# Kernel tuning notes

Measured on AMD Instinct MI355X. Metric: run time of the kernel, lower is better.

Reference implementation:

```python
import jax, jax.numpy as jnp
import numpy as np

# --- static config (matches init_kwargs) ---
B, N, M = 128, 32, 32
C_IMG, NUM_HIDDEN, NUM_CLASSES = 1, 16, 3
INPUT_DIM = C_IMG + NUM_HIDDEN + NUM_CLASSES          # 20
OUT_DIM = NUM_HIDDEN + NUM_CLASSES + 2                # 21 (moving -> 2 action channels)
C_STATE = INPUT_DIM - C_IMG                           # 19
N_NEO, M_NEO = N - 2, M - 2                           # size_neo=None -> N-2
N_ACTIVE, M_ACTIVE = N - 2, M - 2
ITERATIONS = 10
IN_FEAT = 9 * INPUT_DIM + 2                           # 182, position='current'
THRESH = 0.0007


def setup_inputs() -> dict:
    key = jax.random.key(0)
    ks = jax.random.split(key, 7)
    images = jax.random.uniform(ks[0], (B, N, M, C_IMG), dtype=jnp.float32)
    W1 = jax.random.normal(ks[1], (IN_FEAT, 30), dtype=jnp.float32) * 0.08
    b1 = jnp.zeros((30,), jnp.float32)
    W2 = jax.random.normal(ks[2], (30, 30), dtype=jnp.float32) * 0.18
    b2 = jnp.zeros((30,), jnp.float32)
    W3 = jax.random.normal(ks[3], (30, OUT_DIM), dtype=jnp.float32) * 0.18
    b3 = jnp.zeros((OUT_DIM,), jnp.float32)
    return {"images": images, "W1": W1, "b1": b1, "W2": W2, "b2": b2, "W3": W3, "b3": b3}


def _custom_round(a):
    # positive -> +1, negative -> -1 (with deadzone |a| <= 0.0007 -> 0)
    return jnp.where(a > THRESH, 1, jnp.where(a < -THRESH, -1, 0)).astype(jnp.int32)


def _run(images, W1, b1, W2, b2, W3, b3):
    dx = jnp.arange(3)
    b_idx = jnp.arange(B)[:, None, None, None, None]        # (B,1,1,1,1)
    # fixed 3x3 windows into state (comms): state[x:x+3, y:y+3]
    sr = (jnp.arange(N_NEO)[:, None] + dx)[:, None, :, None]  # (Nn,1,3,1)
    sc = (jnp.arange(M_NEO)[:, None] + dx)[None, :, None, :]  # (1,Mn,1,3)
    half_n = N // 2
    half_m = M // 2

    # initial perception matrix: identity grid (N_neo == N_active)
    gx, gy = jnp.meshgrid(jnp.arange(N_NEO), jnp.arange(M_NEO), indexing="ij")
    perc0 = jnp.broadcast_to(jnp.stack([gx, gy], -1).astype(jnp.int32), (B, N_NEO, M_NEO, 2))
    state0 = jnp.zeros((B, N, M, C_STATE), jnp.float32)
    guesses0 = jnp.zeros((B * N_NEO * M_NEO, OUT_DIM), jnp.float32)

    def step(carry, _):
        state, perc, _ = carry
        px = perc[..., 0]  # (B,Nn,Mn) int32
        py = perc[..., 1]
        # dynamic 3x3 image patches at (px, py)
        rows = px[..., None, None] + dx[:, None]            # (B,Nn,Mn,3,1)
        cols = py[..., None, None] + dx[None, :]            # (B,Nn,Mn,1,3)
        perc_patch = images[b_idx, rows, cols, :]           # (B,Nn,Mn,3,3,C_IMG)
        comms = state[:, sr, sc, :]                          # (B,Nn,Mn,3,3,C_STATE)
        feat = jnp.concatenate([perc_patch, comms], axis=-1)  # (B,Nn,Mn,3,3,INPUT_DIM)
        feat = feat.reshape(B * N_NEO * M_NEO, 9 * INPUT_DIM)
        # position='current' features
        pos_x = ((px - half_n) / half_n).astype(jnp.float32).reshape(-1, 1)
        pos_y = ((py - half_m) / half_m).astype(jnp.float32).reshape(-1, 1)
        inp = jnp.concatenate([feat, pos_x, pos_y], axis=-1)  # (B*Nn*Mn, 182)
        h = jax.nn.relu(inp @ W1 + b1)
        h = jax.nn.relu(h @ W2 + b2)
        guesses = h @ W3 + b3                                 # (B*Nn*Mn, 21)
        outputs = guesses.reshape(B, N_NEO, M_NEO, OUT_DIM)
        state = state.at[:, 1:1 + N_NEO, 1:1 + M_NEO, :].add(outputs[..., :C_STATE])
        # movement: round actions to {-1,0,1}, add, clip to [0, N_active-1]
        delta = _custom_round(outputs[..., -2:])
        perc = jnp.clip(perc + delta, 0, N_ACTIVE - 1)
        return (state, perc, guesses), None

    (state, perc, guesses), _ = jax.lax.scan(step, (state0, perc0, guesses0), None, length=ITERATIONS)
    class_state = state[:, 1:1 + N_NEO, 1:1 + M_NEO, -NUM_CLASSES:]
    return class_state, guesses


def reference(images, W1, b1, W2, b2, W3, b3):
    return _run(images, W1, b1, W2, b2, W3, b3)
```

## Files before the change

### kernel.cpp

```cpp
#include <hip/hip_runtime.h>

#define B_      128
#define NPIX    32
#define NNEO    30
#define CSTATE  19
#define CPAD    20
#define OUTD    21
#define ITERS   10
#define THRESHV 0.0007f

#define STATE_ELEMS_PAD (B_ * NPIX * NPIX * CPAD)
#define NCELLS      (B_ * NNEO * NNEO)
#define CLASS_ELEMS (NCELLS * 3)
#define HSTRIDE 31

__global__ void nca_init(float* __restrict__ stateA, float* __restrict__ stateB) {
    int idx = blockIdx.x * blockDim.x + threadIdx.x;
    const int total = B_ * 124 * CPAD;
    if (idx >= total) return;
    int c  = idx % CPAD;
    int t2 = idx / CPAD;
    int cell = t2 % 124;
    int b    = t2 / 124;
    int i, j;
    if (cell < 32)      { i = 0;  j = cell; }
    else if (cell < 64) { i = 31; j = cell - 32; }
    else { int k = cell - 64; i = 1 + (k >> 1); j = (k & 1) ? 31 : 0; }
    size_t off = (((size_t)b * NPIX + i) * NPIX + j) * CPAD + c;
    stateA[off] = 0.0f;
    stateB[off] = 0.0f;
}

__global__ __launch_bounds__(1024, 8)
void nca_step0(const float* __restrict__ img,
               const float* __restrict__ W1, const float* __restrict__ b1,
               const float* __restrict__ W2, const float* __restrict__ b2,
               const float* __restrict__ W3, const float* __restrict__ b3,
               float* __restrict__ state_new, int* __restrict__ perc) {
    __shared__ float s_img[NPIX * NPIX];
    __shared__ float s_h[240 * HSTRIDE];

    const int b   = blockIdx.y;
    const int rg  = blockIdx.x;
    const int i0  = (rg < 2) ? rg * 8 : 16 + (rg - 2) * 7;
    const int nr  = (rg < 2) ? 8 : 7;
    const int tid = threadIdx.x;
    const int qh  = __builtin_amdgcn_readfirstlane(tid >> 8);
    const int cell = tid & 255;
    const int qoff = (qh == 0) ? 0 : (qh == 1) ? 8 : (qh == 2) ? 14 : 22;
    const int off3 = 5 * qh;

    if (tid < NPIX * NPIX / 4) {
        ((float4*)s_img)[tid] = ((const float4*)(img + (size_t)b * NPIX * NPIX))[tid];
    }
    __syncthreads();

    const int cells = nr * NNEO;
    const bool active = cell < cells;

    int r = 0, j = 0, i = 0, gcell = 0, px = 0, py = 0;
    if (active) {
        r = cell / NNEO;
        j = cell % NNEO;
        i = i0 + r;
        gcell = (b * NNEO + i) * NNEO + j;
        px = i; py = j;
    }

    float h1[8];
    {
        const float* __restrict__ bb = b1 + qoff;
#pragma unroll
        for (int q = 0; q < 8; q++) h1[q] = bb[q];
    }
    if (active) {
        for (int pr = 0; pr < 3; pr++) {
            for (int pc = 0; pc < 3; pc++) {
                const int p9 = pr * 3 + pc;
                const float iv = s_img[(px + pr) * NPIX + (py + pc)];
                const float* __restrict__ wp = W1 + (p9 * 20) * 30 + qoff;
#pragma unroll
                for (int q = 0; q < 8; q++) h1[q] += iv * wp[q];
            }
        }
        const float posx = (float)(px - 16) * (1.0f / 16.0f);
        const float posy = (float)(py - 16) * (1.0f / 16.0f);
        const float* __restrict__ wx = W1 + 180 * 30 + qoff;
        const float* __restrict__ wy = W1 + 181 * 30 + qoff;
#pragma unroll
        for (int q = 0; q < 8; q++) h1[q] += posx * wx[q];
#pragma unroll
        for (int q = 0; q < 8; q++) h1[q] += posy * wy[q];
#pragma unroll
        for (int q = 0; q < 8; q++) h1[q] = fmaxf(h1[q], 0.0f);
#pragma unroll
        for (int q = 0; q < 8; q++) s_h[cell * HSTRIDE + qoff + q] = h1[q];
    }
    __syncthreads();

    float h2[8];
    {
        const float* __restrict__ bb = b2 + qoff;
#pragma unroll
        for (int q = 0; q < 8; q++) h2[q] = bb[q];
    }
    if (active) {
        float a1[30];
#pragma unroll
        for (int k = 0; k < 30; k++) a1[k] = s_h[cell * HSTRIDE + k];
        for (int k = 0; k < 30; k++) {
            const float* __restrict__ wr = W2 + k * 30 + qoff;
#pragma unroll
            for (int q = 0; q < 8; q++) h2[q] += a1[k] * wr[q];
        }
#pragma unroll
        for (int q = 0; q < 8; q++) h2[q] = fmaxf(h2[q], 0.0f);
    }
    __syncthreads();
    if (active) {
#pragma unroll
        for (int q = 0; q < 8; q++) s_h[cell * HSTRIDE + qoff + q] = h2[q];
    }
    __syncthreads();

    float o[6];
    {
        const float* __restrict__ bb = b3 + off3;
#pragma unroll
        for (int c = 0; c < 6; c++) o[c] = bb[c];
    }
    if (active) {
        float a2[30];
#pragma unroll
        for (int k = 0; k < 30; k++) a2[k] = s_h[cell * HSTRIDE + k];
        for (int k = 0; k < 30; k++) {
            const float* __restrict__ wr = W3 + k * 21 + off3;
#pragma unroll
            for (int c = 0; c < 6; c++) o[c] += a2[k] * wr[c];
        }
        float* __restrict__ ns =
            state_new + (((size_t)b * NPIX + (i + 1)) * NPIX + (j + 1)) * CPAD;
        if (qh == 0) {
#pragma unroll
            for (int c = 0; c < 6; c++) ns[c] = o[c];
        } else if (qh < 3) {
#pragma unroll
            for (int c = 1; c < 6; c++) ns[off3 + c] = o[c];
        } else {
#pragma unroll
            for (int c = 1; c < 4; c++) ns[15 + c] = o[c];
            int dxm = (o[4] > THRESHV) ? 1 : ((o[4] < -THRESHV) ? -1 : 0);
            int dym = (o[5] > THRESHV) ? 1 : ((o[5] < -THRESHV) ? -1 : 0);
            px += dxm; py += dym;
            px = (px < 0) ? 0 : ((px > NNEO - 1) ? NNEO - 1 : px);
            py = (py < 0) ? 0 : ((py > NNEO - 1) ? NNEO - 1 : py);
            perc[2 * gcell + 0] = px;
            perc[2 * gcell + 1] = py;
        }
    }
}

template<bool LAST>
__global__ __launch_bounds__(1024, 8)
void nca_step(const float* __restrict__ img,
              const float* __restrict__ W1, const float* __restrict__ b1,
              const float* __restrict__ W2, const float* __restrict__ b2,
              const float* __restrict__ W3, const float* __restrict__ b3,
              const float* __restrict__ state_old, float* __restrict__ state_new,
              int* perc, float* __restrict__ guesses_out,
              float* __restrict__ class_out) {
    __shared__ float s_state[10 * NPIX * CPAD];
    __shared__ float s_img[NPIX * NPIX];
    __shared__ float s_h[240 * HSTRIDE];

    const int b   = blockIdx.y;
    const int rg  = blockIdx.x;
    const int i0  = (rg < 2) ? rg * 8 : 16 + (rg - 2) * 7;
    const int nr  = (rg < 2) ? 8 : 7;
    const int tid = threadIdx.x;
    const int qh  = __builtin_amdgcn_readfirstlane(tid >> 8);
    const int cell = tid & 255;
    const int qoff = (qh == 0) ? 0 : (qh == 1) ? 8 : (qh == 2) ? 14 : 22;
    const int off3 = 5 * qh;

    {
        const int n4 = (nr + 2) * NPIX * CPAD / 4;
        const float4* gstate4 =
            (const float4*)(state_old + ((size_t)b * NPIX + i0) * NPIX * CPAD);
        float4* s_state4 = (float4*)s_state;
        for (int t = tid; t < n4; t += 1024) s_state4[t] = gstate4[t];
    }
    if (tid < NPIX * NPIX / 4) {
        ((float4*)s_img)[tid] = ((const float4*)(img + (size_t)b * NPIX * NPIX))[tid];
    }
    __syncthreads();

    const int cells = nr * NNEO;
    const bool active = cell < cells;

    int r = 0, j = 0, i = 0, gcell = 0, px = 0, py = 0;
    if (active) {
        r = cell / NNEO;
        j = cell % NNEO;
        i = i0 + r;
        gcell = (b * NNEO + i) * NNEO + j;
        px = perc[2 * gcell]; py = perc[2 * gcell + 1];
    }

    float h1[8];
    {
        const float* __restrict__ bb = b1 + qoff;
#pragma unroll
        for (int q = 0; q < 8; q++) h1[q] = bb[q];
    }
    if (active) {
        for (int pr = 0; pr < 3; pr++) {
            for (int pc = 0; pc < 3; pc++) {
                const int p9 = pr * 3 + pc;
                const float iv = s_img[(px + pr) * NPIX + (py + pc)];
                const float* __restrict__ wp = W1 + (p9 * 20) * 30 + qoff;
                const int sbase = ((r + pr) * NPIX + (j + pc)) * CPAD;
                float fv[20];
                {
                    const float4* __restrict__ sp =
                        (const float4*)&s_state[sbase];
#pragma unroll
                    for (int v = 0; v < 5; v++)
                        *(float4*)&fv[4 * v] = sp[v];
                }
#pragma unroll
                for (int q = 0; q < 8; q++) h1[q] += iv * wp[q];
                for (int ch = 0; ch < CSTATE; ch++) {
                    const float* __restrict__ wr = wp + (ch + 1) * 30;
#pragma unroll
                    for (int q = 0; q < 8; q++) h1[q] += fv[ch] * wr[q];
                }
            }
        }
        const float posx = (float)(px - 16) * (1.0f / 16.0f);
        const float posy = (float)(py - 16) * (1.0f / 16.0f);
        const float* __restrict__ wx = W1 + 180 * 30 + qoff;
        const float* __restrict__ wy = W1 + 181 * 30 + qoff;
#pragma unroll
        for (int q = 0; q < 8; q++) h1[q] += posx * wx[q];
#pragma unroll
        for (int q = 0; q < 8; q++) h1[q] += posy * wy[q];
#pragma unroll
        for (int q = 0; q < 8; q++) h1[q] = fmaxf(h1[q], 0.0f);
#pragma unroll
        for (int q = 0; q < 8; q++) s_h[cell * HSTRIDE + qoff + q] = h1[q];
    }
    __syncthreads();

    float h2[8];
    {
        const float* __restrict__ bb = b2 + qoff;
#pragma unroll
        for (int q = 0; q < 8; q++) h2[q] = bb[q];
    }
    if (active) {
        float a1[30];
#pragma unroll
        for (int k = 0; k < 30; k++) a1[k] = s_h[cell * HSTRIDE + k];
        for (int k = 0; k < 30; k++) {
            const float* __restrict__ wr = W2 + k * 30 + qoff;
#pragma unroll
            for (int q = 0; q < 8; q++) h2[q] += a1[k] * wr[q];
        }
#pragma unroll
        for (int q = 0; q < 8; q++) h2[q] = fmaxf(h2[q], 0.0f);
    }
    __syncthreads();
    if (active) {
#pragma unroll
        for (int q = 0; q < 8; q++) s_h[cell * HSTRIDE + qoff + q] = h2[q];
    }
    __syncthreads();

    float o[6];
    {
        const float* __restrict__ bb = b3 + off3;
#pragma unroll
        for (int c = 0; c < 6; c++) o[c] = bb[c];
    }
    if (active) {
        float a2[30];
#pragma unroll
        for (int k = 0; k < 30; k++) a2[k] = s_h[cell * HSTRIDE + k];
        for (int k = 0; k < 30; k++) {
            const float* __restrict__ wr = W3 + k * 21 + off3;
#pragma unroll
            for (int c = 0; c < 6; c++) o[c] += a2[k] * wr[c];
        }

        const int lcenter = ((r + 1) * NPIX + (j + 1)) * CPAD;
        if (!LAST) {
            float* __restrict__ ns =
                state_new + (((size_t)b * NPIX + (i + 1)) * NPIX + (j + 1)) * CPAD;
            if (qh == 0) {
#pragma unroll
                for (int c = 0; c < 6; c++)
                    ns[c] = s_state[lcenter + c] + o[c];
            } else if (qh < 3) {
#pragma unroll
                for (int c = 1; c < 6; c++)
                    ns[off3 + c] = s_state[lcenter + off3 + c] + o[c];
            } else {
#pragma unroll
                for (int c = 1; c < 4; c++)
                    ns[15 + c] = s_state[lcenter + 15 + c] + o[c];
                int dxm = (o[4] > THRESHV) ? 1 : ((o[4] < -THRESHV) ? -1 : 0);
                int dym = (o[5] > THRESHV) ? 1 : ((o[5] < -THRESHV) ? -1 : 0);
                px += dxm; py += dym;
                px = (px < 0) ? 0 : ((px > NNEO - 1) ? NNEO - 1 : px);
                py = (py < 0) ? 0 : ((py > NNEO - 1) ? NNEO - 1 : py);
                perc[2 * gcell + 0] = px;
                perc[2 * gcell + 1] = py;
            }
        } else {
            float* __restrict__ g = guesses_out + (size_t)gcell * OUTD;
            if (qh == 0) {
#pragma unroll
                for (int c = 0; c < 6; c++) g[c] = o[c];
            } else {
#pragma unroll
                for (int c = 1; c < 6; c++) g[off3 + c] = o[c];
            }
            if (qh == 3) {
                float* __restrict__ cs = class_out + (size_t)gcell * 3;
#pragma unroll
                for (int cc = 0; cc < 3; cc++)
                    cs[cc] = s_state[lcenter + 16 + cc] + o[1 + cc];
            }
        }
    }
}

extern "C" void kernel_launch(void* const* d_in, const int* in_sizes, int n_in,
                              void* d_out, int out_size, void* d_ws, size_t ws_size,
                              hipStream_t stream) {
    const float* img = (const float*)d_in[0];
    const float* W1  = (const float*)d_in[1];
    const float* b1  = (const float*)d_in[2];
    const float* W2  = (const float*)d_in[3];
    const float* b2  = (const float*)d_in[4];
    const float* W3  = (const float*)d_in[5];
    const float* b3  = (const float*)d_in[6];

    float* out = (float*)d_out;
    float* class_out   = out;
    float* guesses_out = out + CLASS_ELEMS;

    float* stateA = (float*)d_ws;
    float* stateB = stateA + STATE_ELEMS_PAD;
    int*   perc   = (int*)(stateB + STATE_ELEMS_PAD);

    {
        const int total = B_ * 124 * CPAD;
        nca_init<<<(total + 255) / 256, 256, 0, stream>>>(stateA, stateB);
    }

    const dim3 grid(4, B_);
    nca_step0<<<grid, 1024, 0, stream>>>(img, W1, b1, W2, b2, W3, b3,
                                         stateB, perc);
    for (int t = 1; t < ITERS - 1; t++) {
        const float* so = (t & 1) ? stateB : stateA;
        float*       sn = (t & 1) ? stateA : stateB;
        nca_step<false><<<grid, 1024, 0, stream>>>(
            img, W1, b1, W2, b2, W3, b3, so, sn, perc, guesses_out, class_out);
    }
    nca_step<true><<<grid, 1024, 0, stream>>>(
        img, W1, b1, W2, b2, W3, b3, stateB, stateA, perc, guesses_out, class_out);
}
```

Baseline: 346.9 us.

## Compute full MLP per thread, one cell per thread, drop shared memory

Replaces the 1024-thread blocks, which split each cell's 30 hidden units across four thread groups with shared-memory exchange and barriers, by a one-thread-per-cell kernel that computes all 30/30/21 outputs in registers. State windows are read straight from global memory as float4 rather than staged in LDS. Weights are read uniformly from global or scalar memory. This removes the barriers and shared-memory traffic, but raises register pressure to about 90 accumulators per thread and issues redundant overlapping global loads of neighbouring state.

After: 482.7 us. 1.39x slower.

```diff
diff --git a/kernel.cpp b/kernel.cpp
--- a/kernel.cpp
+++ b/kernel.cpp
@@ -12,7 +12,6 @@
 #define STATE_ELEMS_PAD (B_ * NPIX * NPIX * CPAD)
 #define NCELLS      (B_ * NNEO * NNEO)
 #define CLASS_ELEMS (NCELLS * 3)
-#define HSTRIDE 31
 
 __global__ void nca_init(float* __restrict__ stateA, float* __restrict__ stateB) {
     int idx = blockIdx.x * blockDim.x + threadIdx.x;
@@ -20,319 +19,137 @@
     if (idx >= total) return;
     int c  = idx % CPAD;
     int t2 = idx / CPAD;
-    int cell = t2 % 124;
+    int cellp = t2 % 124;
     int b    = t2 / 124;
     int i, j;
-    if (cell < 32)      { i = 0;  j = cell; }
-    else if (cell < 64) { i = 31; j = cell - 32; }
-    else { int k = cell - 64; i = 1 + (k >> 1); j = (k & 1) ? 31 : 0; }
+    if (cellp < 32)      { i = 0;  j = cellp; }
+    else if (cellp < 64) { i = 31; j = cellp - 32; }
+    else { int k = cellp - 64; i = 1 + (k >> 1); j = (k & 1) ? 31 : 0; }
     size_t off = (((size_t)b * NPIX + i) * NPIX + j) * CPAD + c;
     stateA[off] = 0.0f;
     stateB[off] = 0.0f;
 }
 
-__global__ __launch_bounds__(1024, 8)
-void nca_step0(const float* __restrict__ img,
-               const float* __restrict__ W1, const float* __restrict__ b1,
-               const float* __restrict__ W2, const float* __restrict__ b2,
-               const float* __restrict__ W3, const float* __restrict__ b3,
-               float* __restrict__ state_new, int* __restrict__ perc) {
-    __shared__ float s_img[NPIX * NPIX];
-    __shared__ float s_h[240 * HSTRIDE];
+#define L1ROW(x, r) do { const float* __restrict__ wr = wp + (r) * 30; \
+    _Pragma("unroll") for (int o = 0; o < 30; o++) acc[o] += (x) * wr[o]; } while (0)
 
-    const int b   = blockIdx.y;
-    const int rg  = blockIdx.x;
-    const int i0  = (rg < 2) ? rg * 8 : 16 + (rg - 2) * 7;
-    const int nr  = (rg < 2) ? 8 : 7;
-    const int tid = threadIdx.x;
-    const int qh  = __builtin_amdgcn_readfirstlane(tid >> 8);
-    const int cell = tid & 255;
-    const int qoff = (qh == 0) ? 0 : (qh == 1) ? 8 : (qh == 2) ? 14 : 22;
-    const int off3 = 5 * qh;
-
-    if (tid < NPIX * NPIX / 4) {
-        ((float4*)s_img)[tid] = ((const float4*)(img + (size_t)b * NPIX * NPIX))[tid];
-    }
-    __syncthreads();
-
-    const int cells = nr * NNEO;
-    const bool active = cell < cells;
-
-    int r = 0, j = 0, i = 0, gcell = 0, px = 0, py = 0;
-    if (active) {
-        r = cell / NNEO;
-        j = cell % NNEO;
-        i = i0 + r;
-        gcell = (b * NNEO + i) * NNEO + j;
-        px = i; py = j;
-    }
-
-    float h1[8];
-    {
-        const float* __restrict__ bb = b1 + qoff;
-#pragma unroll
-        for (int q = 0; q < 8; q++) h1[q] = bb[q];
-    }
-    if (active) {
-        for (int pr = 0; pr < 3; pr++) {
-            for (int pc = 0; pc < 3; pc++) {
-                const int p9 = pr * 3 + pc;
-                const float iv = s_img[(px + pr) * NPIX + (py + pc)];
-                const float* __restrict__ wp = W1 + (p9 * 20) * 30 + qoff;
-#pragma unroll
-                for (int q = 0; q < 8; q++) h1[q] += iv * wp[q];
-            }
-        }
-        const float posx = (float)(px - 16) * (1.0f / 16.0f);
-        const float posy = (float)(py - 16) * (1.0f / 16.0f);
-        const float* __restrict__ wx = W1 + 180 * 30 + qoff;
-        const float* __restrict__ wy = W1 + 181 * 30 + qoff;
-#pragma unroll
-        for (int q = 0; q < 8; q++) h1[q] += posx * wx[q];
-#pragma unroll
-        for (int q = 0; q < 8; q++) h1[q] += posy * wy[q];
-#pragma unroll
-        for (int q = 0; q < 8; q++) h1[q] = fmaxf(h1[q], 0.0f);
-#pragma unroll
-        for (int q = 0; q < 8; q++) s_h[cell * HSTRIDE + qoff + q] = h1[q];
-    }
-    __syncthreads();
-
-    float h2[8];
-    {
-        const float* __restrict__ bb = b2 + qoff;
-#pragma unroll
-        for (int q = 0; q < 8; q++) h2[q] = bb[q];
-    }
-    if (active) {
-        float a1[30];
-#pragma unroll
-        for (int k = 0; k < 30; k++) a1[k] = s_h[cell * HSTRIDE + k];
-        for (int k = 0; k < 30; k++) {
-            const float* __restrict__ wr = W2 + k * 30 + qoff;
-#pragma unroll
-            for (int q = 0; q < 8; q++) h2[q] += a1[k] * wr[q];
-        }
-#pragma unroll
-        for (int q = 0; q < 8; q++) h2[q] = fmaxf(h2[q], 0.0f);
-    }
-    __syncthreads();
-    if (active) {
-#pragma unroll
-        for (int q = 0; q < 8; q++) s_h[cell * HSTRIDE + qoff + q] = h2[q];
-    }
-    __syncthreads();
-
-    float o[6];
-    {
-        const float* __restrict__ bb = b3 + off3;
-#pragma unroll
-        for (int c = 0; c < 6; c++) o[c] = bb[c];
-    }
-    if (active) {
-        float a2[30];
-#pragma unroll
-        for (int k = 0; k < 30; k++) a2[k] = s_h[cell * HSTRIDE + k];
-        for (int k = 0; k < 30; k++) {
-            const float* __restrict__ wr = W3 + k * 21 + off3;
-#pragma unroll
-            for (int c = 0; c < 6; c++) o[c] += a2[k] * wr[c];
-        }
-        float* __restrict__ ns =
-            state_new + (((size_t)b * NPIX + (i + 1)) * NPIX + (j + 1)) * CPAD;
-        if (qh == 0) {
-#pragma unroll
-            for (int c = 0; c < 6; c++) ns[c] = o[c];
-        } else if (qh < 3) {
-#pragma unroll
-            for (int c = 1; c < 6; c++) ns[off3 + c] = o[c];
-        } else {
-#pragma unroll
-            for (int c = 1; c < 4; c++) ns[15 + c] = o[c];
-            int dxm = (o[4] > THRESHV) ? 1 : ((o[4] < -THRESHV) ? -1 : 0);
-            int dym = (o[5] > THRESHV) ? 1 : ((o[5] < -THRESHV) ? -1 : 0);
-            px += dxm; py += dym;
-            px = (px < 0) ? 0 : ((px > NNEO - 1) ? NNEO - 1 : px);
-            py = (py < 0) ? 0 : ((py > NNEO - 1) ? NNEO - 1 : py);
-            perc[2 * gcell + 0] = px;
-            perc[2 * gcell + 1] = py;
-        }
-    }
-}
-
-template<bool LAST>
-__global__ __launch_bounds__(1024, 8)
-void nca_step(const float* __restrict__ img,
+template<int MODE>
+__global__ __launch_bounds__(256, 2)
+void nca_cell(const float* __restrict__ img,
               const float* __restrict__ W1, const float* __restrict__ b1,
               const float* __restrict__ W2, const float* __restrict__ b2,
               const float* __restrict__ W3, const float* __restrict__ b3,
               const float* __restrict__ state_old, float* __restrict__ state_new,
-              int* perc, float* __restrict__ guesses_out,
-              float* __restrict__ class_out) {
-    __shared__ float s_state[10 * NPIX * CPAD];
-    __shared__ float s_img[NPIX * NPIX];
-    __shared__ float s_h[240 * HSTRIDE];
+              int* __restrict__ perc,
+              float* __restrict__ guesses_out, float* __restrict__ class_out)
+{
+    const int cell = blockIdx.x * 256 + threadIdx.x;
+    const int b  = cell / (NNEO * NNEO);
+    const int ij = cell - b * (NNEO * NNEO);
+    const int i  = ij / NNEO;
+    const int j  = ij - i * NNEO;
 
-    const int b   = blockIdx.y;
-    const int rg  = blockIdx.x;
-    const int i0  = (rg < 2) ? rg * 8 : 16 + (rg - 2) * 7;
-    const int nr  = (rg < 2) ? 8 : 7;
-    const int tid = threadIdx.x;
-    const int qh  = __builtin_amdgcn_readfirstlane(tid >> 8);
-    const int cell = tid & 255;
-    const int qoff = (qh == 0) ? 0 : (qh == 1) ? 8 : (qh == 2) ? 14 : 22;
-    const int off3 = 5 * qh;
+    int px, py;
+    if (MODE == 0) { px = i; py = j; }
+    else           { px = perc[2 * cell]; py = perc[2 * cell + 1]; }
 
+    const float* __restrict__ ib = img + (size_t)b * (NPIX * NPIX);
+
+    float acc[30];
+#pragma unroll
+    for (int o = 0; o < 30; o++) acc[o] = b1[o];
+
+#pragma clang loop unroll(disable)
+    for (int pr = 0; pr < 3; pr++) {
+#pragma clang loop unroll(disable)
+        for (int pc = 0; pc < 3; pc++) {
+            const float iv = ib[(px + pr) * NPIX + (py + pc)];
+            const float* __restrict__ wp = W1 + (pr * 3 + pc) * 20 * 30;
+            if (MODE != 0) {
+                const float4* __restrict__ sp = (const float4*)
+                    (state_old + (((size_t)b * NPIX + (i + pr)) * NPIX + (j + pc)) * CPAD);
+                const float4 f0 = sp[0], f1 = sp[1], f2 = sp[2], f3 = sp[3], f4 = sp[4];
+                L1ROW(iv, 0);
+                L1ROW(f0.x, 1);  L1ROW(f0.y, 2);  L1ROW(f0.z, 3);  L1ROW(f0.w, 4);
+                L1ROW(f1.x, 5);  L1ROW(f1.y, 6);  L1ROW(f1.z, 7);  L1ROW(f1.w, 8);
+                L1ROW(f2.x, 9);  L1ROW(f2.y, 10); L1ROW(f2.z, 11); L1ROW(f2.w, 12);
+                L1ROW(f3.x, 13); L1ROW(f3.y, 14); L1ROW(f3.z, 15); L1ROW(f3.w, 16);
+                L1ROW(f4.x, 17); L1ROW(f4.y, 18); L1ROW(f4.z, 19);
+            } else {
+                L1ROW(iv, 0);
+            }
+        }
+    }
     {
-        const int n4 = (nr + 2) * NPIX * CPAD / 4;
-        const float4* gstate4 =
-            (const float4*)(state_old + ((size_t)b * NPIX + i0) * NPIX * CPAD);
-        float4* s_state4 = (float4*)s_state;
-        for (int t = tid; t < n4; t += 1024) s_state4[t] = gstate4[t];
-    }
-    if (tid < NPIX * NPIX / 4) {
-        ((float4*)s_img)[tid] = ((const float4*)(img + (size_t)b * NPIX * NPIX))[tid];
-    }
-    __syncthreads();
-
-    const int cells = nr * NNEO;
-    const bool active = cell < cells;
-
-    int r = 0, j = 0, i = 0, gcell = 0, px = 0, py = 0;
-    if (active) {
-        r = cell / NNEO;
-        j = cell % NNEO;
-        i = i0 + r;
-        gcell = (b * NNEO + i) * NNEO + j;
-        px = perc[2 * gcell]; py = perc[2 * gcell + 1];
+        const float posx = (float)(px - 16) * 0.0625f;
+        const float posy = (float)(py - 16) * 0.0625f;
+        const float* __restrict__ wp = W1;
+        L1ROW(posx, 180);
+        L1ROW(posy, 181);
     }
 
-    float h1[8];
-    {
-        const float* __restrict__ bb = b1 + qoff;
+    float a1[30];
 #pragma unroll
-        for (int q = 0; q < 8; q++) h1[q] = bb[q];
+    for (int o = 0; o < 30; o++) a1[o] = fmaxf(acc[o], 0.0f);
+
+    float h2[30];
+#pragma unroll
+    for (int o = 0; o < 30; o++) h2[o] = b2[o];
+#pragma unroll
+    for (int k = 0; k < 30; k++) {
+        const float x = a1[k];
+        const float* __restrict__ wr = W2 + k * 30;
+#pragma unroll
+        for (int o = 0; o < 30; o++) h2[o] += x * wr[o];
     }
-    if (active) {
-        for (int pr = 0; pr < 3; pr++) {
-            for (int pc = 0; pc < 3; pc++) {
-                const int p9 = pr * 3 + pc;
-                const float iv = s_img[(px + pr) * NPIX + (py + pc)];
-                const float* __restrict__ wp = W1 + (p9 * 20) * 30 + qoff;
-                const int sbase = ((r + pr) * NPIX + (j + pc)) * CPAD;
-                float fv[20];
-                {
-                    const float4* __restrict__ sp =
-                        (const float4*)&s_state[sbase];
 #pragma unroll
-                    for (int v = 0; v < 5; v++)
-                        *(float4*)&fv[4 * v] = sp[v];
-                }
+    for (int o = 0; o < 30; o++) h2[o] = fmaxf(h2[o], 0.0f);
+
+    float ov[21];
 #pragma unroll
-                for (int q = 0; q < 8; q++) h1[q] += iv * wp[q];
-                for (int ch = 0; ch < CSTATE; ch++) {
-                    const float* __restrict__ wr = wp + (ch + 1) * 30;
+    for (int c = 0; c < 21; c++) ov[c] = b3[c];
 #pragma unroll
-                    for (int q = 0; q < 8; q++) h1[q] += fv[ch] * wr[q];
-                }
-            }
+    for (int k = 0; k < 30; k++) {
+        const float x = h2[k];
+        const float* __restrict__ wr = W3 + k * 21;
+#pragma unroll
+        for (int c = 0; c < 21; c++) ov[c] += x * wr[c];
+    }
+
+    const size_t coff = (((size_t)b * NPIX + (i + 1)) * NPIX + (j + 1)) * CPAD;
+    if (MODE == 2) {
+        float* __restrict__ g = guesses_out + (size_t)cell * OUTD;
+#pragma unroll
+        for (int c = 0; c < 21; c++) g[c] = ov[c];
+        const float4 c4 = *(const float4*)(state_old + coff + 16);
+        float* __restrict__ cs = class_out + (size_t)cell * 3;
+        cs[0] = c4.x + ov[16];
+        cs[1] = c4.y + ov[17];
+        cs[2] = c4.z + ov[18];
+    } else {
+        float4* __restrict__ ns4 = (float4*)(state_new + coff);
+        if (MODE == 0) {
+            ns4[0] = make_float4(ov[0],  ov[1],  ov[2],  ov[3]);
+            ns4[1] = make_float4(ov[4],  ov[5],  ov[6],  ov[7]);
+            ns4[2] = make_float4(ov[8],  ov[9],  ov[10], ov[11]);
+            ns4[3] = make_float4(ov[12], ov[13], ov[14], ov[15]);
+            ns4[4] = make_float4(ov[16], ov[17], ov[18], 0.0f);
+        } else {
+            const float4* __restrict__ cs4 = (const float4*)(state_old + coff);
+            const float4 c0 = cs4[0], c1 = cs4[1], c2 = cs4[2], c3 = cs4[3], c4 = cs4[4];
+            ns4[0] = make_float4(c0.x + ov[0],  c0.y + ov[1],  c0.z + ov[2],  c0.w + ov[3]);
+            ns4[1] = make_float4(c1.x + ov[4],  c1.y + ov[5],  c1.z + ov[6],  c1.w + ov[7]);
+            ns4[2] = make_float4(c2.x + ov[8],  c2.y + ov[9],  c2.z + ov[10], c2.w + ov[11]);
+            ns4[3] = make_float4(c3.x + ov[12], c3.y + ov[13], c3.z + ov[14], c3.w + ov[15]);
+            ns4[4] = make_float4(c4.x + ov[16], c4.y + ov[17], c4.z + ov[18], 0.0f);
         }
-        const float posx = (float)(px - 16) * (1.0f / 16.0f);
-        const float posy = (float)(py - 16) * (1.0f / 16.0f);
-        const float* __restrict__ wx = W1 + 180 * 30 + qoff;
-        const float* __restrict__ wy = W1 + 181 * 30 + qoff;
-#pragma unroll
-        for (int q = 0; q < 8; q++) h1[q] += posx * wx[q];
-#pragma unroll
-        for (int q = 0; q < 8; q++) h1[q] += posy * wy[q];
-#pragma unroll
-        for (int q = 0; q < 8; q++) h1[q] = fmaxf(h1[q], 0.0f);
-#pragma unroll
-        for (int q = 0; q < 8; q++) s_h[cell * HSTRIDE + qoff + q] = h1[q];
-    }
-    __syncthreads();
-
-    float h2[8];
-    {
-        const float* __restrict__ bb = b2 + qoff;
-#pragma unroll
-        for (int q = 0; q < 8; q++) h2[q] = bb[q];
-    }
-    if (active) {
-        float a1[30];
-#pragma unroll
-        for (int k = 0; k < 30; k++) a1[k] = s_h[cell * HSTRIDE + k];
-        for (int k = 0; k < 30; k++) {
-            const float* __restrict__ wr = W2 + k * 30 + qoff;
-#pragma unroll
-            for (int q = 0; q < 8; q++) h2[q] += a1[k] * wr[q];
-        }
-#pragma unroll
-        for (int q = 0; q < 8; q++) h2[q] = fmaxf(h2[q], 0.0f);
-    }
-    __syncthreads();
-    if (active) {
-#pragma unroll
-        for (int q = 0; q < 8; q++) s_h[cell * HSTRIDE + qoff + q] = h2[q];
-    }
-    __syncthreads();
-
-    float o[6];
-    {
-        const float* __restrict__ bb = b3 + off3;
-#pragma unroll
-        for (int c = 0; c < 6; c++) o[c] = bb[c];
-    }
-    if (active) {
-        float a2[30];
-#pragma unroll
-        for (int k = 0; k < 30; k++) a2[k] = s_h[cell * HSTRIDE + k];
-        for (int k = 0; k < 30; k++) {
-            const float* __restrict__ wr = W3 + k * 21 + off3;
-#pragma unroll
-            for (int c = 0; c < 6; c++) o[c] += a2[k] * wr[c];
-        }
-
-        const int lcenter = ((r + 1) * NPIX + (j + 1)) * CPAD;
-        if (!LAST) {
-            float* __restrict__ ns =
-                state_new + (((size_t)b * NPIX + (i + 1)) * NPIX + (j + 1)) * CPAD;
-            if (qh == 0) {
-#pragma unroll
-                for (int c = 0; c < 6; c++)
-                    ns[c] = s_state[lcenter + c] + o[c];
-            } else if (qh < 3) {
-#pragma unroll
-                for (int c = 1; c < 6; c++)
-                    ns[off3 + c] = s_state[lcenter + off3 + c] + o[c];
-            } else {
-#pragma unroll
-                for (int c = 1; c < 4; c++)
-                    ns[15 + c] = s_state[lcenter + 15 + c] + o[c];
-                int dxm = (o[4] > THRESHV) ? 1 : ((o[4] < -THRESHV) ? -1 : 0);
-                int dym = (o[5] > THRESHV) ? 1 : ((o[5] < -THRESHV) ? -1 : 0);
-                px += dxm; py += dym;
-                px = (px < 0) ? 0 : ((px > NNEO - 1) ? NNEO - 1 : px);
-                py = (py < 0) ? 0 : ((py > NNEO - 1) ? NNEO - 1 : py);
-                perc[2 * gcell + 0] = px;
-                perc[2 * gcell + 1] = py;
-            }
-        } else {
-            float* __restrict__ g = guesses_out + (size_t)gcell * OUTD;
-            if (qh == 0) {
-#pragma unroll
-                for (int c = 0; c < 6; c++) g[c] = o[c];
-            } else {
-#pragma unroll
-                for (int c = 1; c < 6; c++) g[off3 + c] = o[c];
-            }
-            if (qh == 3) {
-                float* __restrict__ cs = class_out + (size_t)gcell * 3;
-#pragma unroll
-                for (int cc = 0; cc < 3; cc++)
-                    cs[cc] = s_state[lcenter + 16 + cc] + o[1 + cc];
-            }
-        }
+        int dxm = (ov[19] > THRESHV) ? 1 : ((ov[19] < -THRESHV) ? -1 : 0);
+        int dym = (ov[20] > THRESHV) ? 1 : ((ov[20] < -THRESHV) ? -1 : 0);
+        px += dxm; py += dym;
+        px = (px < 0) ? 0 : ((px > NNEO - 1) ? NNEO - 1 : px);
+        py = (py < 0) ? 0 : ((py > NNEO - 1) ? NNEO - 1 : py);
+        perc[2 * cell + 0] = px;
+        perc[2 * cell + 1] = py;
     }
 }
 
@@ -360,15 +177,18 @@
         nca_init<<<(total + 255) / 256, 256, 0, stream>>>(stateA, stateB);
     }
 
-    const dim3 grid(4, B_);
-    nca_step0<<<grid, 1024, 0, stream>>>(img, W1, b1, W2, b2, W3, b3,
-                                         stateB, perc);
+    const int grid = NCELLS / 256;
+    nca_cell<0><<<grid, 256, 0, stream>>>(img, W1, b1, W2, b2, W3, b3,
+                                          stateA, stateB, perc,
+                                          guesses_out, class_out);
     for (int t = 1; t < ITERS - 1; t++) {
         const float* so = (t & 1) ? stateB : stateA;
         float*       sn = (t & 1) ? stateA : stateB;
-        nca_step<false><<<grid, 1024, 0, stream>>>(
-            img, W1, b1, W2, b2, W3, b3, so, sn, perc, guesses_out, class_out);
+        nca_cell<1><<<grid, 256, 0, stream>>>(img, W1, b1, W2, b2, W3, b3,
+                                              so, sn, perc,
+                                              guesses_out, class_out);
     }
-    nca_step<true><<<grid, 1024, 0, stream>>>(
-        img, W1, b1, W2, b2, W3, b3, stateB, stateA, perc, guesses_out, class_out);
+    nca_cell<2><<<grid, 256, 0, stream>>>(img, W1, b1, W2, b2, W3, b3,
+                                          stateB, stateA, perc,
+                                          guesses_out, class_out);
 }
```
